# Kernel optimization log

Hardware: AMD Instinct MI355X
Metric: run time of the kernel (lower is better)

## Reference

```python
import jax, jax.numpy as jnp
import numpy as np

B, N, D = 32, 2048, 512
K = 64          # cluster_size
G = 16          # ghost_clusters
BN_EPS = 1e-5
L2_EPS = 1e-12


def setup_inputs() -> dict:
    key = jax.random.key(0)
    k1, k2, k3 = jax.random.split(key, 3)
    init_sc = 1.0 / np.sqrt(D)
    x = jax.random.normal(k1, (B, N, D), dtype=jnp.float32)
    clusters = init_sc * jax.random.normal(k2, (D, K + G), dtype=jnp.float32)
    clusters2 = init_sc * jax.random.normal(k3, (D, K), dtype=jnp.float32)
    bn_gamma = jnp.ones((K + G,), dtype=jnp.float32)
    bn_beta = jnp.zeros((K + G,), dtype=jnp.float32)
    return {"x": x, "clusters": clusters, "clusters2": clusters2,
            "bn_gamma": bn_gamma, "bn_beta": bn_beta}


def _l2norm(v, axis):
    n = jnp.sqrt(jnp.sum(v * v, axis=axis, keepdims=True))
    return v / jnp.maximum(n, L2_EPS)


def reference(x, clusters, clusters2, bn_gamma, bn_beta):
    b, n, d = x.shape
    kc = clusters2.shape[1]
    # projection: [B*N, K+G]
    a = x.reshape(-1, d) @ clusters
    # BatchNorm1d (training mode: batch statistics, biased variance)
    mean = jnp.mean(a, axis=0)
    var = jnp.mean((a - mean) ** 2, axis=0)
    a = (a - mean) * jax.lax.rsqrt(var + BN_EPS) * bn_gamma + bn_beta
    # softmax over all clusters, drop ghost clusters
    a = jax.nn.softmax(a, axis=1)[:, :kc].reshape(b, n, kc)
    # fused VLAD: v[b,d,k] = sum_n a[b,n,k] * (x[b,n,d] - c2[d,k])
    a_sum = jnp.sum(a, axis=1)                              # [B, K]
    vlad = jnp.einsum('bnd,bnk->bdk', x, a)                 # [B, D, K]
    vlad = vlad - clusters2[None, :, :] * a_sum[:, None, :]
    # intra-normalize over D, flatten, global L2 normalize
    vlad = _l2norm(vlad, axis=1)
    vlad = vlad.reshape(b, kc * d)
    vlad = _l2norm(vlad, axis=1)
    return vlad
```

## Files before the change

### kernel.cpp

```cpp
#include <hip/hip_runtime.h>
#include <hip/hip_bf16.h>

#define B_ 32
#define N_ 2048
#define D_ 512
#define KC_ 64
#define KG_ 80
#define M_ (B_*N_)

typedef __attribute__((ext_vector_type(8))) short short8;
typedef __attribute__((ext_vector_type(4))) float f32x4;

__device__ __forceinline__ unsigned short bf_rn(float f){
  unsigned int u = __float_as_uint(f);
  unsigned int r = u + 0x7FFFu + ((u >> 16) & 1u);
  return (unsigned short)(r >> 16);
}
__device__ __forceinline__ float bf_up(unsigned short h){
  return __uint_as_float(((unsigned int)h) << 16);
}
__device__ __forceinline__ void cvt8(const float* v, short8& hi, short8& lo){
#pragma unroll
  for (int i=0;i<8;i++){
    unsigned short h = bf_rn(v[i]);
    float rem = v[i] - bf_up(h);
    hi[i] = (short)h;
    lo[i] = (short)bf_rn(rem);
  }
}

__global__ __launch_bounds__(256) void k0_prep(const float* __restrict__ cl,
                                               unsigned short* __restrict__ Bf)
{
  int tid = blockIdx.x*256 + threadIdx.x;
  int l  = tid & 63;
  int hl = (tid >> 6) & 1;
  int j  = (tid >> 7) % 5;
  int c  = tid / 640;
  int kk  = c*32 + (l>>4)*8;
  int col = j*16 + (l&15);
  unsigned short o[8];
#pragma unroll
  for (int jj=0;jj<8;jj++){
    float v = cl[(size_t)(kk+jj)*KG_ + col];
    unsigned short h = bf_rn(v);
    if (hl == 0) o[jj] = h;
    else         o[jj] = bf_rn(v - bf_up(h));
  }
#pragma unroll
  for (int jj=0;jj<8;jj++) Bf[(size_t)tid*8 + jj] = o[jj];
}

__global__ __launch_bounds__(256) void k1_proj(
    const float* __restrict__ x, const unsigned short* __restrict__ Bf,
    float* __restrict__ a, float* __restrict__ S1, float* __restrict__ S2)
{
  __shared__ float ls1[KG_], ls2[KG_];
  const int t = threadIdx.x;
  const int w = t >> 6, lane = t & 63;
  const int m = lane & 15, q = lane >> 4;
  const int row0 = blockIdx.x*64 + w*16;
  if (t < KG_){ ls1[t]=0.f; ls2[t]=0.f; }
  __syncthreads();

  const float* xr = x + (size_t)(row0 + m)*D_ + q*8;

  f32x4 acc[5];
#pragma unroll
  for (int j=0;j<5;j++) acc[j] = (f32x4){0.f,0.f,0.f,0.f};

  float v[8];
  *(float4*)&v[0] = *(const float4*)(xr);
  *(float4*)&v[4] = *(const float4*)(xr + 4);

  for (int c=0;c<16;c++){
    float nv[8];
    if (c < 15){
      *(float4*)&nv[0] = *(const float4*)(xr + (c+1)*32);
      *(float4*)&nv[4] = *(const float4*)(xr + (c+1)*32 + 4);
    }
    const unsigned short* bp = Bf + (size_t)(c*5)*1024 + lane*8;
    short8 bh[5], bl[5];
#pragma unroll
    for (int j=0;j<5;j++){
      bh[j] = *(const short8*)(bp + (size_t)j*1024);
      bl[j] = *(const short8*)(bp + (size_t)j*1024 + 512);
    }
    short8 ah, al;
    cvt8(v, ah, al);
#pragma unroll
    for (int j=0;j<5;j++){
      acc[j] = __builtin_amdgcn_mfma_f32_16x16x32_bf16(ah, bh[j], acc[j], 0,0,0);
      acc[j] = __builtin_amdgcn_mfma_f32_16x16x32_bf16(al, bh[j], acc[j], 0,0,0);
      acc[j] = __builtin_amdgcn_mfma_f32_16x16x32_bf16(ah, bl[j], acc[j], 0,0,0);
    }
    if (c < 15){
#pragma unroll
      for (int i=0;i<8;i++) v[i] = nv[i];
    }
  }

  float s1v[5], s2v[5];
#pragma unroll
  for (int j=0;j<5;j++){
    f32x4 vv = acc[j];
    size_t base = (size_t)(row0 + q*4)*KG_ + j*16 + m;
    a[base]        = vv[0];
    a[base+KG_]    = vv[1];
    a[base+2*KG_]  = vv[2];
    a[base+3*KG_]  = vv[3];
    s1v[j] = vv[0]+vv[1]+vv[2]+vv[3];
    s2v[j] = vv[0]*vv[0]+vv[1]*vv[1]+vv[2]*vv[2]+vv[3]*vv[3];
  }
#pragma unroll
  for (int j=0;j<5;j++){
    float s1 = s1v[j], s2 = s2v[j];
    s1 += __shfl_xor(s1,16); s1 += __shfl_xor(s1,32);
    s2 += __shfl_xor(s2,16); s2 += __shfl_xor(s2,32);
    if (q == 0){
      atomicAdd(&ls1[j*16+m], s1);
      atomicAdd(&ls2[j*16+m], s2);
    }
  }
  __syncthreads();
  if (t < KG_){ atomicAdd(&S1[t], ls1[t]); atomicAdd(&S2[t], ls2[t]); }
}

__global__ void k2_bn(const float* __restrict__ S1, const float* __restrict__ S2,
                      const float* __restrict__ gamma, const float* __restrict__ beta,
                      float* __restrict__ scale, float* __restrict__ shift)
{
  int t = threadIdx.x;
  if (t < KG_){
    const float invM = 1.0f / (float)M_;
    float mean = S1[t] * invM;
    float var  = S2[t] * invM - mean*mean;
    float sc = gamma[t] * rsqrtf(var + 1e-5f);
    scale[t] = sc;
    shift[t] = beta[t] - mean*sc;
  }
}

__global__ __launch_bounds__(256) void k3_softmax(
    float* __restrict__ a, const float* __restrict__ scale,
    const float* __restrict__ shift, float* __restrict__ asum)
{
  __shared__ float as[64*84];
  __shared__ float sc[KG_], sh[KG_];
  __shared__ float lsum[KC_];
  const int t = threadIdx.x;
  const int row0 = blockIdx.x * 64;
  if (t < KG_){ sc[t]=scale[t]; sh[t]=shift[t]; }
  if (t < KC_) lsum[t]=0.f;
  __syncthreads();
#pragma unroll
  for (int l=0;l<20;l++){
    int idx = t + 256*l;
    int r = idx/80, col = idx - r*80;
    float v = a[(size_t)(row0+r)*KG_ + col];
    as[r*84+col] = v*sc[col] + sh[col];
  }
  __syncthreads();
  const int rt = t >> 2;
  const int g  = t & 3;
  float m = -1e30f;
#pragma unroll
  for (int c=0;c<20;c++) m = fmaxf(m, as[rt*84 + g + 4*c]);
  m = fmaxf(m, __shfl_xor(m,1));
  m = fmaxf(m, __shfl_xor(m,2));
  float e[20]; float s = 0.f;
#pragma unroll
  for (int c=0;c<20;c++){ float v = __expf(as[rt*84 + g + 4*c] - m); e[c]=v; s+=v; }
  s += __shfl_xor(s,1);
  s += __shfl_xor(s,2);
  const float inv = 1.f/s;
#pragma unroll
  for (int c=0;c<16;c++){
    int col = g + 4*c;
    float pv = e[c]*inv;
    a[(size_t)(row0+rt)*KG_ + col] = pv;
    float su = pv;
    su += __shfl_xor(su,4);  su += __shfl_xor(su,8);
    su += __shfl_xor(su,16); su += __shfl_xor(su,32);
    if ((t&63) < 4) atomicAdd(&lsum[col], su);
  }
  __syncthreads();
  if (t < KC_) atomicAdd(&asum[(blockIdx.x>>5)*KC_ + t], lsum[t]);
}

__global__ __launch_bounds__(256) void k4_vlad(
    const float* __restrict__ x, const float* __restrict__ p, float* __restrict__ vp)
{
  __shared__ unsigned short xh[2][64*40], xl[2][64*40];
  __shared__ unsigned short ph[2][64*40], pl[2][64*40];
  const int t = threadIdx.x;
  const int blk = blockIdx.x;
  const int ns = blk & 3;
  const int dt = (blk >> 2) & 7;
  const int b  = blk >> 5;
  const int w = t >> 6, lane = t & 63;
  const int m = lane & 15, q = lane >> 4;
  const int d0 = dt*64;
  const int nbase = ns*512;
  const int dloc = t & 63, ng = t >> 6;

  const float* xbase = x + ((size_t)b*N_ + nbase)*D_ + d0 + dloc;
  const float* pbase = p + ((size_t)b*N_ + nbase)*KG_ + dloc;

  f32x4 acc[4];
#pragma unroll
  for (int j=0;j<4;j++) acc[j] = (f32x4){0.f,0.f,0.f,0.f};

  {
    float xv[8], pv[8];
#pragma unroll
    for (int jj=0;jj<8;jj++){
      xv[jj] = xbase[(size_t)(ng*8+jj)*D_];
      pv[jj] = pbase[(size_t)(ng*8+jj)*KG_];
    }
    short8 hi, lo;
    cvt8(xv, hi, lo);
    *(short8*)&xh[0][dloc*40 + ng*8] = hi;
    *(short8*)&xl[0][dloc*40 + ng*8] = lo;
    cvt8(pv, hi, lo);
    *(short8*)&ph[0][dloc*40 + ng*8] = hi;
    *(short8*)&pl[0][dloc*40 + ng*8] = lo;
  }
  __syncthreads();

  for (int ch=0; ch<16; ch++){
    const int cur = ch & 1;
    float nxv[8], npv[8];
    if (ch < 15){
      const float* xp2 = xbase + (size_t)((ch+1)*32)*D_;
      const float* pp2 = pbase + (size_t)((ch+1)*32)*KG_;
#pragma unroll
      for (int jj=0;jj<8;jj++){
        nxv[jj] = xp2[(size_t)(ng*8+jj)*D_];
        npv[jj] = pp2[(size_t)(ng*8+jj)*KG_];
      }
    }
    short8 ahi = *(const short8*)&xh[cur][(w*16+m)*40 + q*8];
    short8 alo = *(const short8*)&xl[cur][(w*16+m)*40 + q*8];
#pragma unroll
    for (int j=0;j<4;j++){
      short8 bhi = *(const short8*)&ph[cur][(j*16+m)*40 + q*8];
      short8 blo = *(const short8*)&pl[cur][(j*16+m)*40 + q*8];
      acc[j] = __builtin_amdgcn_mfma_f32_16x16x32_bf16(ahi, bhi, acc[j], 0,0,0);
      acc[j] = __builtin_amdgcn_mfma_f32_16x16x32_bf16(alo, bhi, acc[j], 0,0,0);
      acc[j] = __builtin_amdgcn_mfma_f32_16x16x32_bf16(ahi, blo, acc[j], 0,0,0);
    }
    if (ch < 15){
      short8 hi, lo;
      cvt8(nxv, hi, lo);
      *(short8*)&xh[cur^1][dloc*40 + ng*8] = hi;
      *(short8*)&xl[cur^1][dloc*40 + ng*8] = lo;
      cvt8(npv, hi, lo);
      *(short8*)&ph[cur^1][dloc*40 + ng*8] = hi;
      *(short8*)&pl[cur^1][dloc*40 + ng*8] = lo;
    }
    __syncthreads();
  }
#pragma unroll
  for (int j=0;j<4;j++){
    f32x4 v = acc[j];
    size_t base = (((size_t)ns*B_ + b)*D_ + d0 + w*16 + q*4)*KC_ + j*16 + m;
    vp[base]         = v[0];
    vp[base +   KC_] = v[1];
    vp[base + 2*KC_] = v[2];
    vp[base + 3*KC_] = v[3];
  }
}

__global__ __launch_bounds__(1024) void k5_norm(
    const float* __restrict__ vp, const float* __restrict__ c2,
    const float* __restrict__ asum, float* __restrict__ out)
{
  __shared__ float part[16][64];
  __shared__ float invd[64];
  __shared__ float gi_s;
  const int b = blockIdx.x;
  const int t = threadIdx.x;
  const int k = t & 63, dg = t >> 6;
  const float av = asum[b*KC_ + k];
  const size_t stride = (size_t)B_*D_*KC_;
  float v[32];
  float ss = 0.f;
#pragma unroll
  for (int s=0;s<32;s++){
    int d = dg + 16*s;
    size_t idx = ((size_t)b*D_ + d)*KC_ + k;
    float vv = 0.f;
#pragma unroll
    for (int nsp=0;nsp<4;nsp++) vv += vp[idx + (size_t)nsp*stride];
    vv -= c2[d*KC_ + k]*av;
    v[s] = vv;
    ss += vv*vv;
  }
  part[dg][k] = ss;
  __syncthreads();
  if (t < 64){
    float n2 = 0.f;
#pragma unroll
    for (int i=0;i<16;i++) n2 += part[i][t];
    float nn = sqrtf(n2);
    float denom = fmaxf(nn, 1e-12f);
    invd[t] = 1.f/denom;
    float ratio = nn/denom;
    float r2 = ratio*ratio;
#pragma unroll
    for (int mm=1;mm<64;mm<<=1) r2 += __shfl_xor(r2, mm);
    if (t==0){
      float g = sqrtf(r2);
      gi_s = 1.f/fmaxf(g, 1e-12f);
    }
  }
  __syncthreads();
  const float gi = gi_s;
  const float ik = invd[k];
#pragma unroll
  for (int s=0;s<32;s++){
    int d = dg + 16*s;
    out[(size_t)b*(D_*KC_) + (size_t)d*KC_ + k] = v[s]*ik*gi;
  }
}

extern "C" void kernel_launch(void* const* d_in, const int* in_sizes, int n_in,
                              void* d_out, int out_size, void* d_ws, size_t ws_size,
                              hipStream_t stream)
{
  const float* x     = (const float*)d_in[0];
  const float* cl    = (const float*)d_in[1];
  const float* c2    = (const float*)d_in[2];
  const float* gamma = (const float*)d_in[3];
  const float* beta  = (const float*)d_in[4];
  float* out = (float*)d_out;
  float* ws  = (float*)d_ws;

  float* S1    = ws;
  float* S2    = ws + 80;
  float* scale = ws + 160;
  float* shift = ws + 240;
  float* asum  = ws + 320;
  unsigned short* Bf = (unsigned short*)(ws + 4096);
  float* a     = ws + 45056;
  float* vp    = a + (size_t)M_*KG_;

  hipMemsetAsync(ws, 0, 2368*sizeof(float), stream);
  k0_prep   <<<40,   256, 0, stream>>>(cl, Bf);
  k1_proj   <<<1024, 256, 0, stream>>>(x, Bf, a, S1, S2);
  k2_bn     <<<1,    128, 0, stream>>>(S1, S2, gamma, beta, scale, shift);
  k3_softmax<<<1024, 256, 0, stream>>>(a, scale, shift, asum);
  k4_vlad   <<<1024, 256, 0, stream>>>(x, a, vp);
  k5_norm   <<<32,  1024, 0, stream>>>(vp, c2, asum, out);
}
```

Baseline: 292.2 us.

## Stage projection weights in LDS, double rows per wave, precompute transposed bf16 softmax

```diff
diff --git a/kernel.cpp b/kernel.cpp
--- a/kernel.cpp
+++ b/kernel.cpp
@@ -47,70 +47,100 @@
     if (hl == 0) o[jj] = h;
     else         o[jj] = bf_rn(v - bf_up(h));
   }
-#pragma unroll
-  for (int jj=0;jj<8;jj++) Bf[(size_t)tid*8 + jj] = o[jj];
+  size_t base = (size_t)c*5120 + (size_t)(j*2+hl)*512 + l*8;
+#pragma unroll
+  for (int jj=0;jj<8;jj++) Bf[base + jj] = o[jj];
 }
 
 __global__ __launch_bounds__(256) void k1_proj(
     const float* __restrict__ x, const unsigned short* __restrict__ Bf,
     float* __restrict__ a, float* __restrict__ S1, float* __restrict__ S2)
 {
+  __shared__ unsigned short Bs[2][5120];
   __shared__ float ls1[KG_], ls2[KG_];
   const int t = threadIdx.x;
   const int w = t >> 6, lane = t & 63;
   const int m = lane & 15, q = lane >> 4;
-  const int row0 = blockIdx.x*64 + w*16;
+  const int rowW = blockIdx.x*128 + w*32;
   if (t < KG_){ ls1[t]=0.f; ls2[t]=0.f; }
-  __syncthreads();
-
-  const float* xr = x + (size_t)(row0 + m)*D_ + q*8;
-
-  f32x4 acc[5];
-#pragma unroll
-  for (int j=0;j<5;j++) acc[j] = (f32x4){0.f,0.f,0.f,0.f};
-
-  float v[8];
-  *(float4*)&v[0] = *(const float4*)(xr);
-  *(float4*)&v[4] = *(const float4*)(xr + 4);
+
+  const float* xr0 = x + (size_t)(rowW + m)*D_ + q*8;
+  const float* xr1 = xr0 + (size_t)16*D_;
+
+  f32x4 acc[2][5];
+#pragma unroll
+  for (int rt=0;rt<2;rt++)
+#pragma unroll
+    for (int j=0;j<5;j++) acc[rt][j] = (f32x4){0.f,0.f,0.f,0.f};
+
+  short8 sreg0, sreg1, sreg2;
+  {
+    const unsigned short* src = Bf;
+    sreg0 = *(const short8*)(src + t*8);
+    sreg1 = *(const short8*)(src + (256+t)*8);
+    if (t < 128) sreg2 = *(const short8*)(src + (512+t)*8);
+    *(short8*)&Bs[0][t*8] = sreg0;
+    *(short8*)&Bs[0][(256+t)*8] = sreg1;
+    if (t < 128) *(short8*)&Bs[0][(512+t)*8] = sreg2;
+  }
+  float v0[8], v1[8], nv0[8], nv1[8];
+  *(float4*)&v0[0] = *(const float4*)(xr0);
+  *(float4*)&v0[4] = *(const float4*)(xr0 + 4);
+  *(float4*)&v1[0] = *(const float4*)(xr1);
+  *(float4*)&v1[4] = *(const float4*)(xr1 + 4);
+  __syncthreads();
 
   for (int c=0;c<16;c++){
-    float nv[8];
+    const int cur = c & 1;
     if (c < 15){
-      *(float4*)&nv[0] = *(const float4*)(xr + (c+1)*32);
-      *(float4*)&nv[4] = *(const float4*)(xr + (c+1)*32 + 4);
-    }
-    const unsigned short* bp = Bf + (size_t)(c*5)*1024 + lane*8;
-    short8 bh[5], bl[5];
+      const unsigned short* src = Bf + (size_t)(c+1)*5120;
+      sreg0 = *(const short8*)(src + t*8);
+      sreg1 = *(const short8*)(src + (256+t)*8);
+      if (t < 128) sreg2 = *(const short8*)(src + (512+t)*8);
+      *(float4*)&nv0[0] = *(const float4*)(xr0 + (c+1)*32);
+      *(float4*)&nv0[4] = *(const float4*)(xr0 + (c+1)*32 + 4);
+      *(float4*)&nv1[0] = *(const float4*)(xr1 + (c+1)*32);
+      *(float4*)&nv1[4] = *(const float4*)(xr1 + (c+1)*32 + 4);
+    }
+    short8 ah0, al0, ah1, al1;
+    cvt8(v0, ah0, al0);
+    cvt8(v1, ah1, al1);
 #pragma unroll
     for (int j=0;j<5;j++){
-      bh[j] = *(const short8*)(bp + (size_t)j*1024);
-      bl[j] = *(const short8*)(bp + (size_t)j*1024 + 512);
-    }
-    short8 ah, al;
-    cvt8(v, ah, al);
+      short8 bh = *(const short8*)&Bs[cur][j*1024 + lane*8];
+      short8 bl = *(const short8*)&Bs[cur][j*1024 + 512 + lane*8];
+      acc[0][j] = __builtin_amdgcn_mfma_f32_16x16x32_bf16(ah0, bh, acc[0][j], 0,0,0);
+      acc[0][j] = __builtin_amdgcn_mfma_f32_16x16x32_bf16(al0, bh, acc[0][j], 0,0,0);
+      acc[0][j] = __builtin_amdgcn_mfma_f32_16x16x32_bf16(ah0, bl, acc[0][j], 0,0,0);
+      acc[1][j] = __builtin_amdgcn_mfma_f32_16x16x32_bf16(ah1, bh, acc[1][j], 0,0,0);
+      acc[1][j] = __builtin_amdgcn_mfma_f32_16x16x32_bf16(al1, bh, acc[1][j], 0,0,0);
+      acc[1][j] = __builtin_amdgcn_mfma_f32_16x16x32_bf16(ah1, bl, acc[1][j], 0,0,0);
+    }
+    if (c < 15){
+      const int nb = cur ^ 1;
+      *(short8*)&Bs[nb][t*8] = sreg0;
+      *(short8*)&Bs[nb][(256+t)*8] = sreg1;
+      if (t < 128) *(short8*)&Bs[nb][(512+t)*8] = sreg2;
+#pragma unroll
+      for (int i=0;i<8;i++){ v0[i]=nv0[i]; v1[i]=nv1[i]; }
+    }
+    __syncthreads();
+  }
+
+  float s1v[5] = {0,0,0,0,0}, s2v[5] = {0,0,0,0,0};
+#pragma unroll
+  for (int rt=0;rt<2;rt++){
 #pragma unroll
     for (int j=0;j<5;j++){
-      acc[j] = __builtin_amdgcn_mfma_f32_16x16x32_bf16(ah, bh[j], acc[j], 0,0,0);
-      acc[j] = __builtin_amdgcn_mfma_f32_16x16x32_bf16(al, bh[j], acc[j], 0,0,0);
-      acc[j] = __builtin_amdgcn_mfma_f32_16x16x32_bf16(ah, bl[j], acc[j], 0,0,0);
-    }
-    if (c < 15){
-#pragma unroll
-      for (int i=0;i<8;i++) v[i] = nv[i];
-    }
-  }
-
-  float s1v[5], s2v[5];
-#pragma unroll
-  for (int j=0;j<5;j++){
-    f32x4 vv = acc[j];
-    size_t base = (size_t)(row0 + q*4)*KG_ + j*16 + m;
-    a[base]        = vv[0];
-    a[base+KG_]    = vv[1];
-    a[base+2*KG_]  = vv[2];
-    a[base+3*KG_]  = vv[3];
-    s1v[j] = vv[0]+vv[1]+vv[2]+vv[3];
-    s2v[j] = vv[0]*vv[0]+vv[1]*vv[1]+vv[2]*vv[2]+vv[3]*vv[3];
+      f32x4 vv = acc[rt][j];
+      size_t base = (size_t)(rowW + rt*16 + q*4)*KG_ + j*16 + m;
+      a[base]        = vv[0];
+      a[base+KG_]    = vv[1];
+      a[base+2*KG_]  = vv[2];
+      a[base+3*KG_]  = vv[3];
+      s1v[j] += vv[0]+vv[1]+vv[2]+vv[3];
+      s2v[j] += vv[0]*vv[0]+vv[1]*vv[1]+vv[2]*vv[2]+vv[3]*vv[3];
+    }
   }
 #pragma unroll
   for (int j=0;j<5;j++){
@@ -142,8 +172,9 @@
 }
 
 __global__ __launch_bounds__(256) void k3_softmax(
-    float* __restrict__ a, const float* __restrict__ scale,
-    const float* __restrict__ shift, float* __restrict__ asum)
+    const float* __restrict__ a, const float* __restrict__ scale,
+    const float* __restrict__ shift, float* __restrict__ asum,
+    unsigned short* __restrict__ pth, unsigned short* __restrict__ ptl)
 {
   __shared__ float as[64*84];
   __shared__ float sc[KG_], sh[KG_];
@@ -163,14 +194,14 @@
   __syncthreads();
   const int rt = t >> 2;
   const int g  = t & 3;
-  float m = -1e30f;
-#pragma unroll
-  for (int c=0;c<20;c++) m = fmaxf(m, as[rt*84 + g + 4*c]);
-  m = fmaxf(m, __shfl_xor(m,1));
-  m = fmaxf(m, __shfl_xor(m,2));
+  float mx = -1e30f;
+#pragma unroll
+  for (int c=0;c<20;c++) mx = fmaxf(mx, as[rt*84 + g + 4*c]);
+  mx = fmaxf(mx, __shfl_xor(mx,1));
+  mx = fmaxf(mx, __shfl_xor(mx,2));
   float e[20]; float s = 0.f;
 #pragma unroll
-  for (int c=0;c<20;c++){ float v = __expf(as[rt*84 + g + 4*c] - m); e[c]=v; s+=v; }
+  for (int c=0;c<20;c++){ float v = __expf(as[rt*84 + g + 4*c] - mx); e[c]=v; s+=v; }
   s += __shfl_xor(s,1);
   s += __shfl_xor(s,2);
   const float inv = 1.f/s;
@@ -178,21 +209,38 @@
   for (int c=0;c<16;c++){
     int col = g + 4*c;
     float pv = e[c]*inv;
-    a[(size_t)(row0+rt)*KG_ + col] = pv;
+    as[rt*84 + col] = pv;
     float su = pv;
     su += __shfl_xor(su,4);  su += __shfl_xor(su,8);
     su += __shfl_xor(su,16); su += __shfl_xor(su,32);
     if ((t&63) < 4) atomicAdd(&lsum[col], su);
   }
   __syncthreads();
+  {
+    const int k = t >> 2, nseg = (t & 3) * 16;
+    const int b = row0 >> 11, n0 = row0 & (N_-1);
+    unsigned short vh[16], vl[16];
+#pragma unroll
+    for (int i=0;i<16;i++){
+      float v = as[(nseg+i)*84 + k];
+      unsigned short h = bf_rn(v);
+      vh[i] = h;
+      vl[i] = bf_rn(v - bf_up(h));
+    }
+    size_t base = ((size_t)b*KC_ + k)*N_ + n0 + nseg;
+    *(short8*)&pth[base]     = *(short8*)&vh[0];
+    *(short8*)&pth[base + 8] = *(short8*)&vh[8];
+    *(short8*)&ptl[base]     = *(short8*)&vl[0];
+    *(short8*)&ptl[base + 8] = *(short8*)&vl[8];
+  }
   if (t < KC_) atomicAdd(&asum[(blockIdx.x>>5)*KC_ + t], lsum[t]);
 }
 
 __global__ __launch_bounds__(256) void k4_vlad(
-    const float* __restrict__ x, const float* __restrict__ p, float* __restrict__ vp)
-{
-  __shared__ unsigned short xh[2][64*40], xl[2][64*40];
-  __shared__ unsigned short ph[2][64*40], pl[2][64*40];
+    const float* __restrict__ x, const unsigned short* __restrict__ pth,
+    const unsigned short* __restrict__ ptl, float* __restrict__ vp)
+{
+  __shared__ unsigned short xh[2][2560], xl[2][2560];
   const int t = threadIdx.x;
   const int blk = blockIdx.x;
   const int ns = blk & 3;
@@ -205,59 +253,56 @@
   const int dloc = t & 63, ng = t >> 6;
 
   const float* xbase = x + ((size_t)b*N_ + nbase)*D_ + d0 + dloc;
-  const float* pbase = p + ((size_t)b*N_ + nbase)*KG_ + dloc;
+  const unsigned short* phb = pth + ((size_t)b*KC_ + m)*N_ + nbase + q*8;
+  const unsigned short* plb = ptl + ((size_t)b*KC_ + m)*N_ + nbase + q*8;
 
   f32x4 acc[4];
 #pragma unroll
   for (int j=0;j<4;j++) acc[j] = (f32x4){0.f,0.f,0.f,0.f};
 
+  short8 pb[4][2], npb[4][2];
+#pragma unroll
+  for (int j=0;j<4;j++){
+    pb[j][0] = *(const short8*)(phb + (size_t)(j*16)*N_);
+    pb[j][1] = *(const short8*)(plb + (size_t)(j*16)*N_);
+  }
   {
-    float xv[8], pv[8];
-#pragma unroll
-    for (int jj=0;jj<8;jj++){
-      xv[jj] = xbase[(size_t)(ng*8+jj)*D_];
-      pv[jj] = pbase[(size_t)(ng*8+jj)*KG_];
-    }
-    short8 hi, lo;
-    cvt8(xv, hi, lo);
+    float xv[8];
+#pragma unroll
+    for (int jj=0;jj<8;jj++) xv[jj] = xbase[(size_t)(ng*8+jj)*D_];
+    short8 hi, lo; cvt8(xv, hi, lo);
     *(short8*)&xh[0][dloc*40 + ng*8] = hi;
     *(short8*)&xl[0][dloc*40 + ng*8] = lo;
-    cvt8(pv, hi, lo);
-    *(short8*)&ph[0][dloc*40 + ng*8] = hi;
-    *(short8*)&pl[0][dloc*40 + ng*8] = lo;
   }
   __syncthreads();
 
   for (int ch=0; ch<16; ch++){
     const int cur = ch & 1;
-    float nxv[8], npv[8];
+    float nxv[8];
     if (ch < 15){
-      const float* xp2 = xbase + (size_t)((ch+1)*32)*D_;
-      const float* pp2 = pbase + (size_t)((ch+1)*32)*KG_;
-#pragma unroll
-      for (int jj=0;jj<8;jj++){
-        nxv[jj] = xp2[(size_t)(ng*8+jj)*D_];
-        npv[jj] = pp2[(size_t)(ng*8+jj)*KG_];
+      const int no = (ch+1)*32;
+#pragma unroll
+      for (int jj=0;jj<8;jj++) nxv[jj] = xbase[(size_t)(no + ng*8+jj)*D_];
+#pragma unroll
+      for (int j=0;j<4;j++){
+        npb[j][0] = *(const short8*)(phb + (size_t)(j*16)*N_ + no);
+        npb[j][1] = *(const short8*)(plb + (size_t)(j*16)*N_ + no);
       }
     }
     short8 ahi = *(const short8*)&xh[cur][(w*16+m)*40 + q*8];
     short8 alo = *(const short8*)&xl[cur][(w*16+m)*40 + q*8];
 #pragma unroll
     for (int j=0;j<4;j++){
-      short8 bhi = *(const short8*)&ph[cur][(j*16+m)*40 + q*8];
-      short8 blo = *(const short8*)&pl[cur][(j*16+m)*40 + q*8];
-      acc[j] = __builtin_amdgcn_mfma_f32_16x16x32_bf16(ahi, bhi, acc[j], 0,0,0);
-      acc[j] = __builtin_amdgcn_mfma_f32_16x16x32_bf16(alo, bhi, acc[j], 0,0,0);
-      acc[j] = __builtin_amdgcn_mfma_f32_16x16x32_bf16(ahi, blo, acc[j], 0,0,0);
+      acc[j] = __builtin_amdgcn_mfma_f32_16x16x32_bf16(ahi, pb[j][0], acc[j], 0,0,0);
+      acc[j] = __builtin_amdgcn_mfma_f32_16x16x32_bf16(alo, pb[j][0], acc[j], 0,0,0);
+      acc[j] = __builtin_amdgcn_mfma_f32_16x16x32_bf16(ahi, pb[j][1], acc[j], 0,0,0);
     }
     if (ch < 15){
-      short8 hi, lo;
-      cvt8(nxv, hi, lo);
+      short8 hi, lo; cvt8(nxv, hi, lo);
       *(short8*)&xh[cur^1][dloc*40 + ng*8] = hi;
       *(short8*)&xl[cur^1][dloc*40 + ng*8] = lo;
-      cvt8(npv, hi, lo);
-      *(short8*)&ph[cur^1][dloc*40 + ng*8] = hi;
-      *(short8*)&pl[cur^1][dloc*40 + ng*8] = lo;
+#pragma unroll
+      for (int j=0;j<4;j++){ pb[j][0]=npb[j][0]; pb[j][1]=npb[j][1]; }
     }
     __syncthreads();
   }
@@ -344,13 +389,15 @@
   float* asum  = ws + 320;
   unsigned short* Bf = (unsigned short*)(ws + 4096);
   float* a     = ws + 45056;
-  float* vp    = a + (size_t)M_*KG_;
+  unsigned short* pth = (unsigned short*)(ws + 5287936);
+  unsigned short* ptl = (unsigned short*)(ws + 7385088);
+  float* vp    = a;
 
   hipMemsetAsync(ws, 0, 2368*sizeof(float), stream);
   k0_prep   <<<40,   256, 0, stream>>>(cl, Bf);
-  k1_proj   <<<1024, 256, 0, stream>>>(x, Bf, a, S1, S2);
+  k1_proj   <<<512,  256, 0, stream>>>(x, Bf, a, S1, S2);
   k2_bn     <<<1,    128, 0, stream>>>(S1, S2, gamma, beta, scale, shift);
-  k3_softmax<<<1024, 256, 0, stream>>>(a, scale, shift, asum);
-  k4_vlad   <<<1024, 256, 0, stream>>>(x, a, vp);
+  k3_softmax<<<1024, 256, 0, stream>>>(a, scale, shift, asum, pth, ptl);
+  k4_vlad   <<<1024, 256, 0, stream>>>(x, pth, ptl, vp);
   k5_norm   <<<32,  1024, 0, stream>>>(vp, c2, asum, out);
 }
```

After: 310.7 us. 1.06x slower.
